# Performance work log

Measured on AMD Instinct MI355X. Metric: run time of the kernel, lower is better.

The kernel has to match this reference:

```python
import jax, jax.numpy as jnp
import numpy as np

B, C, CI, T, H, W = 2, 1024, 512, 32, 14, 14
N = T * H * W


def setup_inputs() -> dict:
    key = jax.random.key(0)
    ks = jax.random.split(key, 6)
    s_in = 1.0 / np.sqrt(C)
    s_mid = 1.0 / np.sqrt(CI)
    return {
        "x": jax.random.normal(ks[0], (B, C, T, H, W), jnp.float32),
        "Wk": jax.random.normal(ks[1], (CI, C), jnp.float32) * s_in,
        "bk": jnp.zeros((CI,), jnp.float32),
        "Wq": jax.random.normal(ks[2], (CI, C), jnp.float32) * s_in,
        "bq": jnp.zeros((CI,), jnp.float32),
        "Wv": jax.random.normal(ks[3], (CI, C), jnp.float32) * s_in,
        "bv": jnp.zeros((CI,), jnp.float32),
        "Wo": jax.random.normal(ks[4], (C, CI), jnp.float32) * s_mid,
        "bo": jnp.zeros((C,), jnp.float32),
    }


def reference(x, Wk, bk, Wq, bq, Wv, bv, Wo, bo):
    # x: (B, C, T, H, W). Dropout layers are identity at inference.
    b, c, t, h, w = x.shape
    n = t * h * w
    xf = x.reshape(b, c, n)                          # (B, C, N)
    k = jnp.einsum("dc,bcn->bdn", Wk, xf) + bk[None, :, None]   # (B, CI, N)
    q = jnp.einsum("dc,bcn->bdn", Wq, xf) + bq[None, :, None]   # (B, CI, N)
    v = jnp.einsum("dc,bcn->bdn", Wv, xf) + bv[None, :, None]   # (B, CI, N)
    # alpha[b,i,j] = sum_d key[b,i,d] * query[b,d,j], scaled by 1/T
    alpha = jnp.einsum("bdi,bdj->bij", k, q) / float(t)          # (B, N, N)
    alpha = jax.nn.softmax(alpha, axis=-1)
    # y (B, CI, N) with y[b,c,i] = sum_j alpha[b,i,j] * v[b,c,j]
    y = jnp.einsum("bij,bcj->bci", alpha, v)
    out = jnp.einsum("dc,bcn->bdn", Wo, y) + bo[None, :, None]   # (B, C, N)
    return out.reshape(b, c, t, h, w) + x
```

## Files before the change

### kernel.cpp

```cpp
#include <hip/hip_runtime.h>

#define Bb 2
#define Cc 1024
#define CIi 512
#define Nn 6272
#define JH 3136
#define SCALE (1.0f / 32.0f)

typedef __bf16 bf16;
typedef __bf16 bf16x8 __attribute__((ext_vector_type(8)));
typedef float f32x4 __attribute__((ext_vector_type(4)));
typedef unsigned int u32;
typedef unsigned char u8;
typedef unsigned int u32x4 __attribute__((ext_vector_type(4)));

__device__ __forceinline__ void g2l16(const void* g, void* l) {
  __builtin_amdgcn_global_load_lds(
      (const __attribute__((address_space(1))) u32*)g,
      (__attribute__((address_space(3))) u32*)(size_t)l, 16, 0, 0);
}

__device__ __forceinline__ u8 to_fp8(float v) {
  return (u8)(__builtin_amdgcn_cvt_pk_fp8_f32(v, v, 0, 0) & 0xff);
}

__global__ __launch_bounds__(256) void xpose_kernel(const float* __restrict__ x,
                                                    bf16* __restrict__ xT) {
  __shared__ float tile[32][33];
  int b = blockIdx.z;
  int n0 = blockIdx.x * 32, c0 = blockIdx.y * 32;
  int tn = threadIdx.x & 31, tr = threadIdx.x >> 5;
  const float* xp = x + ((size_t)b * Cc + c0) * Nn + n0;
  for (int i = 0; i < 4; i++) {
    int c = tr + i * 8;
    tile[c][tn] = xp[(size_t)c * Nn + tn];
  }
  __syncthreads();
  bf16* op = xT + ((size_t)b * Nn + n0) * Cc + c0;
  for (int i = 0; i < 4; i++) {
    int n = tr + i * 8;
    op[(size_t)n * Cc + tn] = (bf16)tile[tn][n];
  }
}

__global__ __launch_bounds__(256) void proj_kernel(
    const bf16* __restrict__ xT, const float* __restrict__ Wk,
    const float* __restrict__ Wq, const float* __restrict__ Wv,
    const float* __restrict__ bk, const float* __restrict__ bq,
    const float* __restrict__ bv, u8* __restrict__ kT8, u8* __restrict__ qT8,
    bf16* __restrict__ vv) {
  int z = blockIdx.z;
  int b = z / 3, proj = z % 3;
  const float* W = proj == 0 ? Wk : (proj == 1 ? Wq : Wv);
  const float* bias = proj == 0 ? bk : (proj == 1 ? bq : bv);
  int m0 = blockIdx.x * 128;
  int d0 = blockIdx.y * 128;
  __shared__ __align__(16) bf16 la[128 * 40];
  __shared__ __align__(16) bf16 lb[128 * 40];
  int tid = threadIdx.x;
  int wave = tid >> 6, lane = tid & 63, quad = lane >> 4, l16 = lane & 15;
  int wm = (wave >> 1) * 64, wn = (wave & 1) * 64;
  int row2 = tid >> 1, half = tid & 1;

  f32x4 acc[4][4] = {};
  const bf16* aSrc = xT + ((size_t)b * Nn + m0) * Cc;
  const float* bSrc = W + (size_t)(d0 + row2) * Cc;

  for (int k0 = 0; k0 < Cc; k0 += 32) {
    const u32x4* ga = (const u32x4*)(aSrc + (size_t)row2 * Cc + k0 + half * 16);
    u32x4 a0 = ga[0], a1 = ga[1];
    const f32x4* gb = (const f32x4*)(bSrc + k0 + half * 16);
    f32x4 w0 = gb[0], w1 = gb[1], w2 = gb[2], w3 = gb[3];
    *(u32x4*)&la[row2 * 40 + half * 16] = a0;
    *(u32x4*)&la[row2 * 40 + half * 16 + 8] = a1;
    bf16x8 p0 = {(bf16)w0[0], (bf16)w0[1], (bf16)w0[2], (bf16)w0[3],
                 (bf16)w1[0], (bf16)w1[1], (bf16)w1[2], (bf16)w1[3]};
    bf16x8 p1 = {(bf16)w2[0], (bf16)w2[1], (bf16)w2[2], (bf16)w2[3],
                 (bf16)w3[0], (bf16)w3[1], (bf16)w3[2], (bf16)w3[3]};
    *(bf16x8*)&lb[row2 * 40 + half * 16] = p0;
    *(bf16x8*)&lb[row2 * 40 + half * 16 + 8] = p1;
    __syncthreads();
    bf16x8 af[4], bfr[4];
    for (int t = 0; t < 4; t++)
      af[t] = *(const bf16x8*)&la[(wm + t * 16 + l16) * 40 + quad * 8];
    for (int t = 0; t < 4; t++)
      bfr[t] = *(const bf16x8*)&lb[(wn + t * 16 + l16) * 40 + quad * 8];
    for (int tm = 0; tm < 4; tm++)
      for (int tn = 0; tn < 4; tn++)
        acc[tm][tn] = __builtin_amdgcn_mfma_f32_16x16x32_bf16(
            af[tm], bfr[tn], acc[tm][tn], 0, 0, 0);
    __syncthreads();
  }
  for (int tn = 0; tn < 4; tn++) {
    int dcol = d0 + wn + tn * 16 + l16;
    float bval = bias[dcol];
    for (int tm = 0; tm < 4; tm++) {
      int nbase = m0 + wm + tm * 16 + quad * 4;
      for (int r = 0; r < 4; r++) {
        float val = acc[tm][tn][r] + bval;
        int nrow = nbase + r;
        if (proj == 0) {
          kT8[((size_t)b * Nn + nrow) * CIi + dcol] = to_fp8(val);
        } else if (proj == 1) {
          int ch = (dcol >> 3) ^ (nrow & 15);
          qT8[((size_t)b * Nn + nrow) * CIi + ch * 8 + (dcol & 7)] =
              to_fp8(val);
        } else {
          vv[((size_t)b * CIi + dcol) * Nn + nrow] = (bf16)val;
        }
      }
    }
  }
}

__global__ __launch_bounds__(512, 2) void attn_kernel(
    const u8* __restrict__ kT8, const u8* __restrict__ qT8,
    const bf16* __restrict__ vv, bf16* __restrict__ yp,
    float* __restrict__ ml) {
  int l = blockIdx.x;
  int jh = l & 1, b = (l >> 1) & 1;
  int i0 = (l >> 2) * 128;
  int tid = threadIdx.x;
  int wave = tid >> 6, lane = tid & 63, quad = lane >> 4, l16 = lane & 15;
  int dw = wave * 64;

  __shared__ __align__(16) u8 lq[2][64 * 512];
  __shared__ __align__(16) bf16 Psm[128 * 72];
  __shared__ float redi[128];

  const u8* qb = qT8 + ((size_t)b * Nn + (size_t)jh * JH) * CIi;
  const bf16* vb = vv + (size_t)b * CIi * Nn + (size_t)jh * JH;

  long kf[16];
  {
    const u8* kp = kT8 + ((size_t)b * Nn + i0 + wave * 16 + l16) * CIi +
                   quad * 8;
#pragma unroll
    for (int kk = 0; kk < 16; kk++)
      kf[kk] = *(const long*)(kp + kk * 32);
  }
  f32x4 oacc[8][4] = {};
  f32x4 l_acc = {};

  {
    const u8* qrow = qb + (size_t)(wave * 8) * CIi + lane * 16;
#pragma unroll
    for (int r = 0; r < 4; r++)
      g2l16(qrow + r * 1024, &lq[0][(wave * 8) * 512 + r * 1024]);
  }
  __syncthreads();

  for (int j0 = 0; j0 < JH; j0 += 64) {
    int t = (j0 >> 6) & 1;
    u32x4 vf[2][4];
#pragma unroll
    for (int jc = 0; jc < 2; jc++)
#pragma unroll
      for (int ds = 0; ds < 4; ds++)
        vf[jc][ds] = *(const u32x4*)(vb + (size_t)(dw + ds * 16 + l16) * Nn +
                                     j0 + jc * 32 + quad * 8);
    __builtin_amdgcn_sched_barrier(0);
    if (j0 + 64 < JH) {
      const u8* qrow = qb + (size_t)(j0 + 64 + wave * 8) * CIi + lane * 16;
#pragma unroll
      for (int r = 0; r < 4; r++)
        g2l16(qrow + r * 1024, &lq[t ^ 1][(wave * 8) * 512 + r * 1024]);
    }
    f32x4 s[4] = {};
    {
      const u8* q0 = &lq[t][l16 * 512];
#pragma unroll
      for (int kk = 0; kk < 16; kk++) {
        int sl = ((kk * 4 + quad) ^ l16) * 8;
        long qf0 = *(const long*)(q0 + sl);
        long qf1 = *(const long*)(q0 + 16 * 512 + sl);
        long qf2 = *(const long*)(q0 + 32 * 512 + sl);
        long qf3 = *(const long*)(q0 + 48 * 512 + sl);
        s[0] = __builtin_amdgcn_mfma_f32_16x16x32_fp8_fp8(kf[kk], qf0, s[0],
                                                          0, 0, 0);
        s[1] = __builtin_amdgcn_mfma_f32_16x16x32_fp8_fp8(kf[kk], qf1, s[1],
                                                          0, 0, 0);
        s[2] = __builtin_amdgcn_mfma_f32_16x16x32_fp8_fp8(kf[kk], qf2, s[2],
                                                          0, 0, 0);
        s[3] = __builtin_amdgcn_mfma_f32_16x16x32_fp8_fp8(kf[kk], qf3, s[3],
                                                          0, 0, 0);
      }
    }
    {
#pragma unroll
      for (int jb = 0; jb < 4; jb++)
#pragma unroll
        for (int r = 0; r < 4; r++) {
          float p = __expf(fminf(fmaf(s[jb][r], SCALE, -2.0f), 20.0f));
          l_acc[r] += p;
          int gi = wave * 16 + quad * 4 + r;
          int gj = jb * 16 + l16;
          Psm[gi * 72 + gj] = (bf16)p;
        }
    }
    asm volatile("s_waitcnt lgkmcnt(0)" ::: "memory");
    __builtin_amdgcn_s_barrier();
    asm volatile("" ::: "memory");

#pragma unroll
    for (int jc = 0; jc < 2; jc++)
#pragma unroll
      for (int is = 0; is < 8; is++) {
        bf16x8 pf = *(const bf16x8*)&Psm[(is * 16 + l16) * 72 + jc * 32 +
                                         quad * 8];
#pragma unroll
        for (int ds = 0; ds < 4; ds++)
          oacc[is][ds] = __builtin_amdgcn_mfma_f32_16x16x32_bf16(
              pf, __builtin_bit_cast(bf16x8, vf[jc][ds]), oacc[is][ds], 0, 0,
              0);
      }
    __syncthreads();
  }

#pragma unroll
  for (int o = 1; o < 16; o <<= 1)
#pragma unroll
    for (int r = 0; r < 4; r++) l_acc[r] += __shfl_xor(l_acc[r], o);
  if (l16 == 0) {
#pragma unroll
    for (int r = 0; r < 4; r++) {
      int gi = wave * 16 + quad * 4 + r;
      ml[(size_t)(jh * Bb + b) * Nn + i0 + gi] = l_acc[r];
      redi[gi] = 1.0f / l_acc[r];
    }
  }
  __syncthreads();
  bf16* ypb = yp + ((size_t)jh * Bb + b) * Nn * CIi;
#pragma unroll
  for (int is = 0; is < 8; is++) {
    f32x4 inv = *(const f32x4*)&redi[is * 16 + quad * 4];
#pragma unroll
    for (int ds = 0; ds < 4; ds++)
#pragma unroll
      for (int r = 0; r < 4; r++)
        ypb[(size_t)(i0 + is * 16 + quad * 4 + r) * CIi + dw + ds * 16 + l16] =
            (bf16)(oacc[is][ds][r] * inv[r]);
  }
}

__global__ __launch_bounds__(256) void merge_kernel(const bf16* __restrict__ yp,
                                                    const float* __restrict__ ml,
                                                    bf16* __restrict__ y) {
  int idx = blockIdx.x * 256 + threadIdx.x;
  int row = idx >> 6, c = idx & 63;
  float l0 = ml[row];
  float l1 = ml[(size_t)Bb * Nn + row];
  float inv = 1.0f / (l0 + l1);
  float w0 = l0 * inv, w1 = l1 * inv;
  bf16x8 v0 = *(const bf16x8*)&yp[(size_t)row * CIi + c * 8];
  bf16x8 v1 =
      *(const bf16x8*)&yp[(size_t)Bb * Nn * CIi + (size_t)row * CIi + c * 8];
  bf16x8 o;
#pragma unroll
  for (int k = 0; k < 8; k++)
    o[k] = (bf16)(w0 * (float)v0[k] + w1 * (float)v1[k]);
  *(bf16x8*)&y[(size_t)row * CIi + c * 8] = o;
}

__global__ __launch_bounds__(256) void out_kernel(
    const bf16* __restrict__ y, const float* __restrict__ Wo,
    const float* __restrict__ bo, const float* __restrict__ x,
    float* __restrict__ out) {
  int b = blockIdx.z;
  int d0 = blockIdx.x * 128;
  int m0 = blockIdx.y * 128;
  __shared__ __align__(16) bf16 la[128 * 40];
  __shared__ __align__(16) bf16 lb[128 * 40];
  int tid = threadIdx.x;
  int wave = tid >> 6, lane = tid & 63, quad = lane >> 4, l16 = lane & 15;
  int wm = (wave >> 1) * 64, wn = (wave & 1) * 64;
  int row2 = tid >> 1, half = tid & 1;
  f32x4 acc[4][4] = {};
  const float* aSrc = Wo + (size_t)(d0 + row2) * CIi;
  const bf16* bSrc = y + ((size_t)b * Nn + m0 + row2) * CIi;
  for (int k0 = 0; k0 < CIi; k0 += 32) {
    const f32x4* ga = (const f32x4*)(aSrc + k0 + half * 16);
    f32x4 w0 = ga[0], w1 = ga[1], w2 = ga[2], w3 = ga[3];
    const u32x4* gb = (const u32x4*)(bSrc + k0 + half * 16);
    u32x4 b0 = gb[0], b1 = gb[1];
    bf16x8 p0 = {(bf16)w0[0], (bf16)w0[1], (bf16)w0[2], (bf16)w0[3],
                 (bf16)w1[0], (bf16)w1[1], (bf16)w1[2], (bf16)w1[3]};
    bf16x8 p1 = {(bf16)w2[0], (bf16)w2[1], (bf16)w2[2], (bf16)w2[3],
                 (bf16)w3[0], (bf16)w3[1], (bf16)w3[2], (bf16)w3[3]};
    *(bf16x8*)&la[row2 * 40 + half * 16] = p0;
    *(bf16x8*)&la[row2 * 40 + half * 16 + 8] = p1;
    *(u32x4*)&lb[row2 * 40 + half * 16] = b0;
    *(u32x4*)&lb[row2 * 40 + half * 16 + 8] = b1;
    __syncthreads();
    bf16x8 af[4], bfr[4];
    for (int t = 0; t < 4; t++)
      af[t] = *(const bf16x8*)&la[(wm + t * 16 + l16) * 40 + quad * 8];
    for (int t = 0; t < 4; t++)
      bfr[t] = *(const bf16x8*)&lb[(wn + t * 16 + l16) * 40 + quad * 8];
    for (int tm = 0; tm < 4; tm++)
      for (int tn = 0; tn < 4; tn++)
        acc[tm][tn] = __builtin_amdgcn_mfma_f32_16x16x32_bf16(
            af[tm], bfr[tn], acc[tm][tn], 0, 0, 0);
    __syncthreads();
  }
  for (int tm = 0; tm < 4; tm++) {
    for (int r = 0; r < 4; r++) {
      int drow = d0 + wm + tm * 16 + quad * 4 + r;
      float bval = bo[drow];
      const float* xrow = x + ((size_t)b * Cc + drow) * Nn;
      float* orow = out + ((size_t)b * Cc + drow) * Nn;
      for (int tn = 0; tn < 4; tn++) {
        int ncol = m0 + wn + tn * 16 + l16;
        orow[ncol] = acc[tm][tn][r] + bval + xrow[ncol];
      }
    }
  }
}

extern "C" void kernel_launch(void* const* d_in, const int* in_sizes, int n_in,
                              void* d_out, int out_size, void* d_ws,
                              size_t ws_size, hipStream_t stream) {
  (void)in_sizes;
  (void)n_in;
  (void)out_size;
  (void)ws_size;
  const float* x = (const float*)d_in[0];
  const float* Wk = (const float*)d_in[1];
  const float* bk = (const float*)d_in[2];
  const float* Wq = (const float*)d_in[3];
  const float* bq = (const float*)d_in[4];
  const float* Wv = (const float*)d_in[5];
  const float* bv = (const float*)d_in[6];
  const float* Wo = (const float*)d_in[7];
  const float* bo = (const float*)d_in[8];
  float* out = (float*)d_out;

  bf16* xT = (bf16*)d_ws;
  bf16* yp = (bf16*)d_ws;
  bf16* y = (bf16*)d_ws + (size_t)Bb * Nn * Cc;
  u8* kT8 = (u8*)d_out;
  u8* qT8 = kT8 + (size_t)Bb * Nn * CIi;
  bf16* vv = (bf16*)(qT8 + (size_t)Bb * Nn * CIi);
  float* ml = (float*)((char*)d_out + (size_t)40 * 1024 * 1024);

  xpose_kernel<<<dim3(Nn / 32, Cc / 32, Bb), 256, 0, stream>>>(x, xT);
  proj_kernel<<<dim3(Nn / 128, CIi / 128, 3 * Bb), 256, 0, stream>>>(
      xT, Wk, Wq, Wv, bk, bq, bv, kT8, qT8, vv);
  attn_kernel<<<dim3((Nn / 128) * 2 * Bb), 512, 0, stream>>>(kT8, qT8, vv, yp,
                                                             ml);
  merge_kernel<<<dim3(Bb * Nn * 64 / 256), 256, 0, stream>>>(yp, ml, y);
  out_kernel<<<dim3(Cc / 128, Nn / 128, Bb), 256, 0, stream>>>(y, Wo, bo, x,
                                                               out);
}
```

Measured before the change: 520.0 us.

## Split attention block across 16 waves partitioning key and channel dims

Doubles the attention block to 1024 threads, arranging waves as 8 row groups by 2 key halves, with each wave owning half as many output channels. Softmax row sums are combined across the two key-half waves through shared memory before normalization. The aim is lower per-wave register pressure and more waves to hide latency. In exchange, K fragment loads are duplicated, P reads from LDS per MFMA increase, and the launch bound (1024,4) may force register spills.

```diff
diff --git a/kernel.cpp b/kernel.cpp
--- a/kernel.cpp
+++ b/kernel.cpp
@@ -113,7 +113,7 @@
   }
 }
 
-__global__ __launch_bounds__(512, 2) void attn_kernel(
+__global__ __launch_bounds__(1024, 4) void attn_kernel(
     const u8* __restrict__ kT8, const u8* __restrict__ qT8,
     const bf16* __restrict__ vv, bf16* __restrict__ yp,
     float* __restrict__ ml) {
@@ -122,10 +122,12 @@
   int i0 = (l >> 2) * 128;
   int tid = threadIdx.x;
   int wave = tid >> 6, lane = tid & 63, quad = lane >> 4, l16 = lane & 15;
-  int dw = wave * 64;
+  int wi = wave & 7, wj = wave >> 3;
+  int dw = wave * 32;
 
   __shared__ __align__(16) u8 lq[2][64 * 512];
   __shared__ __align__(16) bf16 Psm[128 * 72];
+  __shared__ float redw[2][128];
   __shared__ float redi[128];
 
   const u8* qb = qT8 + ((size_t)b * Nn + (size_t)jh * JH) * CIi;
@@ -133,68 +135,63 @@
 
   long kf[16];
   {
-    const u8* kp = kT8 + ((size_t)b * Nn + i0 + wave * 16 + l16) * CIi +
+    const u8* kp = kT8 + ((size_t)b * Nn + i0 + wi * 16 + l16) * CIi +
                    quad * 8;
 #pragma unroll
     for (int kk = 0; kk < 16; kk++)
       kf[kk] = *(const long*)(kp + kk * 32);
   }
-  f32x4 oacc[8][4] = {};
+  f32x4 oacc[8][2] = {};
   f32x4 l_acc = {};
 
   {
-    const u8* qrow = qb + (size_t)(wave * 8) * CIi + lane * 16;
-#pragma unroll
-    for (int r = 0; r < 4; r++)
-      g2l16(qrow + r * 1024, &lq[0][(wave * 8) * 512 + r * 1024]);
+    const u8* qrow = qb + (size_t)(wave * 4) * CIi + lane * 16;
+#pragma unroll
+    for (int r = 0; r < 2; r++)
+      g2l16(qrow + r * 1024, &lq[0][(wave * 4) * 512 + r * 1024]);
   }
   __syncthreads();
 
   for (int j0 = 0; j0 < JH; j0 += 64) {
     int t = (j0 >> 6) & 1;
-    u32x4 vf[2][4];
+    u32x4 vf[2][2];
 #pragma unroll
     for (int jc = 0; jc < 2; jc++)
 #pragma unroll
-      for (int ds = 0; ds < 4; ds++)
+      for (int ds = 0; ds < 2; ds++)
         vf[jc][ds] = *(const u32x4*)(vb + (size_t)(dw + ds * 16 + l16) * Nn +
                                      j0 + jc * 32 + quad * 8);
     __builtin_amdgcn_sched_barrier(0);
     if (j0 + 64 < JH) {
-      const u8* qrow = qb + (size_t)(j0 + 64 + wave * 8) * CIi + lane * 16;
-#pragma unroll
-      for (int r = 0; r < 4; r++)
-        g2l16(qrow + r * 1024, &lq[t ^ 1][(wave * 8) * 512 + r * 1024]);
-    }
-    f32x4 s[4] = {};
+      const u8* qrow = qb + (size_t)(j0 + 64 + wave * 4) * CIi + lane * 16;
+#pragma unroll
+      for (int r = 0; r < 2; r++)
+        g2l16(qrow + r * 1024, &lq[t ^ 1][(wave * 4) * 512 + r * 1024]);
+    }
+    f32x4 s[2] = {};
     {
-      const u8* q0 = &lq[t][l16 * 512];
+      const u8* q0 = &lq[t][(wj * 32 + l16) * 512];
+      const u8* q1 = q0 + 16 * 512;
 #pragma unroll
       for (int kk = 0; kk < 16; kk++) {
         int sl = ((kk * 4 + quad) ^ l16) * 8;
         long qf0 = *(const long*)(q0 + sl);
-        long qf1 = *(const long*)(q0 + 16 * 512 + sl);
-        long qf2 = *(const long*)(q0 + 32 * 512 + sl);
-        long qf3 = *(const long*)(q0 + 48 * 512 + sl);
+        long qf1 = *(const long*)(q1 + sl);
         s[0] = __builtin_amdgcn_mfma_f32_16x16x32_fp8_fp8(kf[kk], qf0, s[0],
                                                           0, 0, 0);
         s[1] = __builtin_amdgcn_mfma_f32_16x16x32_fp8_fp8(kf[kk], qf1, s[1],
                                                           0, 0, 0);
-        s[2] = __builtin_amdgcn_mfma_f32_16x16x32_fp8_fp8(kf[kk], qf2, s[2],
-                                                          0, 0, 0);
-        s[3] = __builtin_amdgcn_mfma_f32_16x16x32_fp8_fp8(kf[kk], qf3, s[3],
-                                                          0, 0, 0);
       }
     }
     {
 #pragma unroll
-      for (int jb = 0; jb < 4; jb++)
+      for (int jb = 0; jb < 2; jb++)
 #pragma unroll
         for (int r = 0; r < 4; r++) {
           float p = __expf(fminf(fmaf(s[jb][r], SCALE, -2.0f), 20.0f));
           l_acc[r] += p;
-          int gi = wave * 16 + quad * 4 + r;
-          int gj = jb * 16 + l16;
+          int gi = wi * 16 + quad * 4 + r;
+          int gj = wj * 32 + jb * 16 + l16;
           Psm[gi * 72 + gj] = (bf16)p;
         }
     }
@@ -209,7 +206,7 @@
         bf16x8 pf = *(const bf16x8*)&Psm[(is * 16 + l16) * 72 + jc * 32 +
                                          quad * 8];
 #pragma unroll
-        for (int ds = 0; ds < 4; ds++)
+        for (int ds = 0; ds < 2; ds++)
           oacc[is][ds] = __builtin_amdgcn_mfma_f32_16x16x32_bf16(
               pf, __builtin_bit_cast(bf16x8, vf[jc][ds]), oacc[is][ds], 0, 0,
               0);
@@ -223,11 +220,14 @@
     for (int r = 0; r < 4; r++) l_acc[r] += __shfl_xor(l_acc[r], o);
   if (l16 == 0) {
 #pragma unroll
-    for (int r = 0; r < 4; r++) {
-      int gi = wave * 16 + quad * 4 + r;
-      ml[(size_t)(jh * Bb + b) * Nn + i0 + gi] = l_acc[r];
-      redi[gi] = 1.0f / l_acc[r];
-    }
+    for (int r = 0; r < 4; r++)
+      redw[wj][wi * 16 + quad * 4 + r] = l_acc[r];
+  }
+  __syncthreads();
+  if (tid < 128) {
+    float s = redw[0][tid] + redw[1][tid];
+    ml[(size_t)(jh * Bb + b) * Nn + i0 + tid] = s;
+    redi[tid] = 1.0f / s;
   }
   __syncthreads();
   bf16* ypb = yp + ((size_t)jh * Bb + b) * Nn * CIi;
@@ -235,7 +235,7 @@
   for (int is = 0; is < 8; is++) {
     f32x4 inv = *(const f32x4*)&redi[is * 16 + quad * 4];
 #pragma unroll
-    for (int ds = 0; ds < 4; ds++)
+    for (int ds = 0; ds < 2; ds++)
 #pragma unroll
       for (int r = 0; r < 4; r++)
         ypb[(size_t)(i0 + is * 16 + quad * 4 + r) * CIi + dw + ds * 16 + l16] =
@@ -346,8 +346,8 @@
   xpose_kernel<<<dim3(Nn / 32, Cc / 32, Bb), 256, 0, stream>>>(x, xT);
   proj_kernel<<<dim3(Nn / 128, CIi / 128, 3 * Bb), 256, 0, stream>>>(
       xT, Wk, Wq, Wv, bk, bq, bv, kT8, qT8, vv);
-  attn_kernel<<<dim3((Nn / 128) * 2 * Bb), 512, 0, stream>>>(kT8, qT8, vv, yp,
-                                                             ml);
+  attn_kernel<<<dim3((Nn / 128) * 2 * Bb), 1024, 0, stream>>>(kT8, qT8, vv, yp,
+                                                              ml);
   merge_kernel<<<dim3(Bb * Nn * 64 / 256), 256, 0, stream>>>(yp, ml, y);
   out_kernel<<<dim3(Cc / 128, Nn / 128, Bb), 256, 0, stream>>>(y, Wo, bo, x,
                                                                out);
```

New measurement: 652.7 us. 1.26x slower.

## Double-buffer LDS tiles with register prefetch in projection and output GEMMs

Applied to the files above, without the earlier changes.

The projection and output GEMM kernels now use two LDS buffers. Each step loads the next K-slice from global memory into registers while the MFMAs consume the current slice, then writes that slice to the other buffer. This removes one barrier per iteration and hides global-load latency behind compute. The cost is twice the shared memory and more live registers, which may lower occupancy.

```diff
diff --git a/kernel.cpp b/kernel.cpp
--- a/kernel.cpp
+++ b/kernel.cpp
@@ -55,41 +55,72 @@
   const float* bias = proj == 0 ? bk : (proj == 1 ? bq : bv);
   int m0 = blockIdx.x * 128;
   int d0 = blockIdx.y * 128;
-  __shared__ __align__(16) bf16 la[128 * 40];
-  __shared__ __align__(16) bf16 lb[128 * 40];
+  __shared__ __align__(16) bf16 la[2][128 * 40];
+  __shared__ __align__(16) bf16 lb[2][128 * 40];
   int tid = threadIdx.x;
   int wave = tid >> 6, lane = tid & 63, quad = lane >> 4, l16 = lane & 15;
   int wm = (wave >> 1) * 64, wn = (wave & 1) * 64;
   int row2 = tid >> 1, half = tid & 1;
 
   f32x4 acc[4][4] = {};
-  const bf16* aSrc = xT + ((size_t)b * Nn + m0) * Cc;
-  const float* bSrc = W + (size_t)(d0 + row2) * Cc;
-
-  for (int k0 = 0; k0 < Cc; k0 += 32) {
-    const u32x4* ga = (const u32x4*)(aSrc + (size_t)row2 * Cc + k0 + half * 16);
-    u32x4 a0 = ga[0], a1 = ga[1];
-    const f32x4* gb = (const f32x4*)(bSrc + k0 + half * 16);
-    f32x4 w0 = gb[0], w1 = gb[1], w2 = gb[2], w3 = gb[3];
-    *(u32x4*)&la[row2 * 40 + half * 16] = a0;
-    *(u32x4*)&la[row2 * 40 + half * 16 + 8] = a1;
+  const bf16* aSrc = xT + ((size_t)b * Nn + m0 + row2) * Cc + half * 16;
+  const float* bSrc = W + (size_t)(d0 + row2) * Cc + half * 16;
+
+  u32x4 a0, a1;
+  f32x4 w0, w1, w2, w3;
+  {
+    const u32x4* ga = (const u32x4*)aSrc;
+    a0 = ga[0];
+    a1 = ga[1];
+    const f32x4* gb = (const f32x4*)bSrc;
+    w0 = gb[0]; w1 = gb[1]; w2 = gb[2]; w3 = gb[3];
+  }
+  {
+    *(u32x4*)&la[0][row2 * 40 + half * 16] = a0;
+    *(u32x4*)&la[0][row2 * 40 + half * 16 + 8] = a1;
     bf16x8 p0 = {(bf16)w0[0], (bf16)w0[1], (bf16)w0[2], (bf16)w0[3],
                  (bf16)w1[0], (bf16)w1[1], (bf16)w1[2], (bf16)w1[3]};
     bf16x8 p1 = {(bf16)w2[0], (bf16)w2[1], (bf16)w2[2], (bf16)w2[3],
                  (bf16)w3[0], (bf16)w3[1], (bf16)w3[2], (bf16)w3[3]};
-    *(bf16x8*)&lb[row2 * 40 + half * 16] = p0;
-    *(bf16x8*)&lb[row2 * 40 + half * 16 + 8] = p1;
-    __syncthreads();
+    *(bf16x8*)&lb[0][row2 * 40 + half * 16] = p0;
+    *(bf16x8*)&lb[0][row2 * 40 + half * 16 + 8] = p1;
+  }
+  __syncthreads();
+
+  const int NSTEP = Cc / 32;
+  for (int step = 0; step < NSTEP; step++) {
+    int cur = step & 1;
+    if (step + 1 < NSTEP) {
+      const u32x4* ga = (const u32x4*)(aSrc + (step + 1) * 32);
+      a0 = ga[0];
+      a1 = ga[1];
+      const f32x4* gb = (const f32x4*)(bSrc + (step + 1) * 32);
+      w0 = gb[0]; w1 = gb[1]; w2 = gb[2]; w3 = gb[3];
+    }
     bf16x8 af[4], bfr[4];
+#pragma unroll
     for (int t = 0; t < 4; t++)
-      af[t] = *(const bf16x8*)&la[(wm + t * 16 + l16) * 40 + quad * 8];
+      af[t] = *(const bf16x8*)&la[cur][(wm + t * 16 + l16) * 40 + quad * 8];
+#pragma unroll
     for (int t = 0; t < 4; t++)
-      bfr[t] = *(const bf16x8*)&lb[(wn + t * 16 + l16) * 40 + quad * 8];
+      bfr[t] = *(const bf16x8*)&lb[cur][(wn + t * 16 + l16) * 40 + quad * 8];
+#pragma unroll
     for (int tm = 0; tm < 4; tm++)
+#pragma unroll
       for (int tn = 0; tn < 4; tn++)
         acc[tm][tn] = __builtin_amdgcn_mfma_f32_16x16x32_bf16(
             af[tm], bfr[tn], acc[tm][tn], 0, 0, 0);
-    __syncthreads();
+    if (step + 1 < NSTEP) {
+      *(u32x4*)&la[cur ^ 1][row2 * 40 + half * 16] = a0;
+      *(u32x4*)&la[cur ^ 1][row2 * 40 + half * 16 + 8] = a1;
+      bf16x8 p0 = {(bf16)w0[0], (bf16)w0[1], (bf16)w0[2], (bf16)w0[3],
+                   (bf16)w1[0], (bf16)w1[1], (bf16)w1[2], (bf16)w1[3]};
+      bf16x8 p1 = {(bf16)w2[0], (bf16)w2[1], (bf16)w2[2], (bf16)w2[3],
+                   (bf16)w3[0], (bf16)w3[1], (bf16)w3[2], (bf16)w3[3]};
+      *(bf16x8*)&lb[cur ^ 1][row2 * 40 + half * 16] = p0;
+      *(bf16x8*)&lb[cur ^ 1][row2 * 40 + half * 16 + 8] = p1;
+      __syncthreads();
+    }
   }
   for (int tn = 0; tn < 4; tn++) {
     int dcol = d0 + wn + tn * 16 + l16;
@@ -269,39 +300,71 @@
   int b = blockIdx.z;
   int d0 = blockIdx.x * 128;
   int m0 = blockIdx.y * 128;
-  __shared__ __align__(16) bf16 la[128 * 40];
-  __shared__ __align__(16) bf16 lb[128 * 40];
+  __shared__ __align__(16) bf16 la[2][128 * 40];
+  __shared__ __align__(16) bf16 lb[2][128 * 40];
   int tid = threadIdx.x;
   int wave = tid >> 6, lane = tid & 63, quad = lane >> 4, l16 = lane & 15;
   int wm = (wave >> 1) * 64, wn = (wave & 1) * 64;
   int row2 = tid >> 1, half = tid & 1;
   f32x4 acc[4][4] = {};
-  const float* aSrc = Wo + (size_t)(d0 + row2) * CIi;
-  const bf16* bSrc = y + ((size_t)b * Nn + m0 + row2) * CIi;
-  for (int k0 = 0; k0 < CIi; k0 += 32) {
-    const f32x4* ga = (const f32x4*)(aSrc + k0 + half * 16);
-    f32x4 w0 = ga[0], w1 = ga[1], w2 = ga[2], w3 = ga[3];
-    const u32x4* gb = (const u32x4*)(bSrc + k0 + half * 16);
-    u32x4 b0 = gb[0], b1 = gb[1];
+  const float* aSrc = Wo + (size_t)(d0 + row2) * CIi + half * 16;
+  const bf16* bSrc = y + ((size_t)b * Nn + m0 + row2) * CIi + half * 16;
+
+  f32x4 w0, w1, w2, w3;
+  u32x4 b0, b1;
+  {
+    const f32x4* ga = (const f32x4*)aSrc;
+    w0 = ga[0]; w1 = ga[1]; w2 = ga[2]; w3 = ga[3];
+    const u32x4* gb = (const u32x4*)bSrc;
+    b0 = gb[0];
+    b1 = gb[1];
+  }
+  {
     bf16x8 p0 = {(bf16)w0[0], (bf16)w0[1], (bf16)w0[2], (bf16)w0[3],
                  (bf16)w1[0], (bf16)w1[1], (bf16)w1[2], (bf16)w1[3]};
     bf16x8 p1 = {(bf16)w2[0], (bf16)w2[1], (bf16)w2[2], (bf16)w2[3],
                  (bf16)w3[0], (bf16)w3[1], (bf16)w3[2], (bf16)w3[3]};
-    *(bf16x8*)&la[row2 * 40 + half * 16] = p0;
-    *(bf16x8*)&la[row2 * 40 + half * 16 + 8] = p1;
-    *(u32x4*)&lb[row2 * 40 + half * 16] = b0;
-    *(u32x4*)&lb[row2 * 40 + half * 16 + 8] = b1;
-    __syncthreads();
+    *(bf16x8*)&la[0][row2 * 40 + half * 16] = p0;
+    *(bf16x8*)&la[0][row2 * 40 + half * 16 + 8] = p1;
+    *(u32x4*)&lb[0][row2 * 40 + half * 16] = b0;
+    *(u32x4*)&lb[0][row2 * 40 + half * 16 + 8] = b1;
+  }
+  __syncthreads();
+
+  const int NSTEP = CIi / 32;
+  for (int step = 0; step < NSTEP; step++) {
+    int cur = step & 1;
+    if (step + 1 < NSTEP) {
+      const f32x4* ga = (const f32x4*)(aSrc + (step + 1) * 32);
+      w0 = ga[0]; w1 = ga[1]; w2 = ga[2]; w3 = ga[3];
+      const u32x4* gb = (const u32x4*)(bSrc + (step + 1) * 32);
+      b0 = gb[0];
+      b1 = gb[1];
+    }
     bf16x8 af[4], bfr[4];
+#pragma unroll
     for (int t = 0; t < 4; t++)
-      af[t] = *(const bf16x8*)&la[(wm + t * 16 + l16) * 40 + quad * 8];
+      af[t] = *(const bf16x8*)&la[cur][(wm + t * 16 + l16) * 40 + quad * 8];
+#pragma unroll
     for (int t = 0; t < 4; t++)
-      bfr[t] = *(const bf16x8*)&lb[(wn + t * 16 + l16) * 40 + quad * 8];
+      bfr[t] = *(const bf16x8*)&lb[cur][(wn + t * 16 + l16) * 40 + quad * 8];
+#pragma unroll
     for (int tm = 0; tm < 4; tm++)
+#pragma unroll
       for (int tn = 0; tn < 4; tn++)
         acc[tm][tn] = __builtin_amdgcn_mfma_f32_16x16x32_bf16(
             af[tm], bfr[tn], acc[tm][tn], 0, 0, 0);
-    __syncthreads();
+    if (step + 1 < NSTEP) {
+      bf16x8 p0 = {(bf16)w0[0], (bf16)w0[1], (bf16)w0[2], (bf16)w0[3],
+                   (bf16)w1[0], (bf16)w1[1], (bf16)w1[2], (bf16)w1[3]};
+      bf16x8 p1 = {(bf16)w2[0], (bf16)w2[1], (bf16)w2[2], (bf16)w2[3],
+                   (bf16)w3[0], (bf16)w3[1], (bf16)w3[2], (bf16)w3[3]};
+      *(bf16x8*)&la[cur ^ 1][row2 * 40 + half * 16] = p0;
+      *(bf16x8*)&la[cur ^ 1][row2 * 40 + half * 16 + 8] = p1;
+      *(u32x4*)&lb[cur ^ 1][row2 * 40 + half * 16] = b0;
+      *(u32x4*)&lb[cur ^ 1][row2 * 40 + half * 16 + 8] = b1;
+      __syncthreads();
+    }
   }
   for (int tm = 0; tm < 4; tm++) {
     for (int r = 0; r < 4; r++) {
```

After: 483.9 us. 1.07x faster.
